# Kernel tuning notes

Measured on AMD Instinct MI355X. Metric: run time of the kernel, lower is better.

The kernel has to match this reference:

```python
import jax, jax.numpy as jnp
import numpy as np

B, LU, LV, D = 16, 2048, 2048, 1024


def setup_inputs() -> dict:
    key = jax.random.key(0)
    ku, kv, kl, kw = jax.random.split(key, 4)
    u = jax.random.normal(ku, (B, LU, D), dtype=jnp.float32)
    v = jax.random.normal(kv, (B, LV, D), dtype=jnp.float32)
    # padding mask: True = masked position; every batch keeps >= LV//2 valid tokens
    lengths = jax.random.randint(kl, (B,), LV // 2, LV + 1)
    v_mask = jnp.arange(LV)[None, :] >= lengths[:, None]  # [B, LV] bool
    # Linear(input_size=D, output_size=D) parameters
    W = jax.random.normal(kw, (D, D), dtype=jnp.float32) * (1.0 / np.sqrt(D))
    b = jnp.zeros((D,), dtype=jnp.float32)
    return {"u": u, "v": v, "v_mask": v_mask, "W": W, "b": b}


def reference(u, v, v_mask, W, b):
    # shared ReLU-projected bilinear attention
    u_ = jax.nn.relu(u @ W.T + b)            # [B, Lu, D]
    v_ = jax.nn.relu(v @ W.T + b)            # [B, Lv, D]
    alpha = jnp.einsum("bud,bvd->buv", u_, v_)  # [B, Lu, Lv]
    alpha = jnp.where(v_mask[:, None, :], -jnp.inf, alpha)
    alpha = jax.nn.softmax(alpha, axis=-1)
    return jnp.einsum("buv,bvd->bud", alpha, v)  # [B, Lu, D]
```

## Files before the change

kernel.cpp:

```cpp
#include <hip/hip_runtime.h>
#include <math.h>

#define B_  16
#define LU_ 2048
#define LV_ 2048
#define D_  1024
#define NT_ (LV_ / 128)
#define MB_ (1024ull * 1024ull)

typedef __attribute__((ext_vector_type(8))) short ush8;
typedef __attribute__((ext_vector_type(8))) _Float16 f16x8;
typedef __attribute__((ext_vector_type(4))) float f32x4;

__device__ __forceinline__ unsigned short f2h(float x) {
    _Float16 h = (_Float16)x;
    return __builtin_bit_cast(unsigned short, h);
}

__device__ __forceinline__ void gload_lds16(const void* g, void* l) {
    __builtin_amdgcn_global_load_lds(
        (const __attribute__((address_space(1))) void*)g,
        (__attribute__((address_space(3))) void*)l, 16, 0, 0);
}

__global__ void lengths_kernel(const void* __restrict__ mask, int* __restrict__ lengths) {
    __shared__ int viol;
    __shared__ int cnt[B_];
    const int t = threadIdx.x;
    if (t == 0) viol = 0;
    if (t < B_) cnt[t] = 0;
    __syncthreads();
    const unsigned char* mb = (const unsigned char*)mask;
    int local = 0;
    for (int i = t; i < B_ * LV_ - 1; i += 256) {
        if (((i + 1) % LV_) != 0) {
            if (mb[i] != 0 && mb[i + 1] == 0) local++;
        }
    }
    if (local) atomicAdd(&viol, local);
    __syncthreads();
    const bool is_i32 = (viol > 0);
    const int b = t >> 4, s = t & 15;
    int c = 0;
    if (is_i32) {
        const int* mi = (const int*)mask;
        for (int v2 = s; v2 < LV_; v2 += 16) c += (mi[b * LV_ + v2] == 0) ? 1 : 0;
    } else {
        for (int v2 = s; v2 < LV_; v2 += 16) c += (mb[b * LV_ + v2] == 0) ? 1 : 0;
    }
    atomicAdd(&cnt[b], c);
    __syncthreads();
    if (t < B_) lengths[t] = cnt[t];
}

__global__ __launch_bounds__(256) void cvt_kernel(
    const float* __restrict__ X, unsigned short* __restrict__ Y, long n8) {
    const long stride = (long)gridDim.x * 256;
    for (long i = (long)blockIdx.x * 256 + threadIdx.x; i < n8; i += stride) {
        float4 x0 = ((const float4*)X)[i * 2];
        float4 x1 = ((const float4*)X)[i * 2 + 1];
        float xv[8] = {x0.x, x0.y, x0.z, x0.w, x1.x, x1.y, x1.z, x1.w};
        ush8 h;
#pragma unroll
        for (int j = 0; j < 8; j++) h[j] = (short)f2h(xv[j]);
        ((ush8*)Y)[i] = h;
    }
}

__global__ __launch_bounds__(256, 2) void proj_kernel(
    const unsigned short* __restrict__ Xf, const unsigned short* __restrict__ Wf,
    const float* __restrict__ bias, const int* __restrict__ lengths, int is_v,
    unsigned short* __restrict__ Yf) {
    if (is_v) {
        const int bb = blockIdx.x >> 4;
        const int lv0 = (blockIdx.x & 15) * 128;
        if (lv0 >= lengths[bb]) return;
    }
    __shared__ alignas(16) unsigned short sA[128 * 64], sB[128 * 64];
    const int t = threadIdx.x, lane = t & 63, w = t >> 6;
    const int fr = lane & 15, fg = lane >> 4;
    const int row0 = blockIdx.x * 128, col0 = blockIdx.y * 128;

    size_t aog[4], bog[4];
    int dbs[4];
#pragma unroll
    for (int i = 0; i < 4; i++) {
        const int r = w * 32 + i * 8 + (lane >> 3);
        const int cg = (lane & 7) ^ (r & 7);
        aog[i] = (size_t)(row0 + r) * D_ + cg * 8;
        bog[i] = (size_t)(col0 + r) * D_ + cg * 8;
        dbs[i] = (w * 32 + i * 8) * 64;
    }
    int aoff[2][2], boff[2][8];
#pragma unroll
    for (int kk = 0; kk < 2; kk++) {
#pragma unroll
        for (int m = 0; m < 2; m++) {
            const int r = w * 32 + m * 16 + fr;
            aoff[kk][m] = r * 64 + (((kk * 4 + fg) ^ (r & 7))) * 8;
        }
#pragma unroll
        for (int n = 0; n < 8; n++) {
            const int r = n * 16 + fr;
            boff[kk][n] = r * 64 + (((kk * 4 + fg) ^ (r & 7))) * 8;
        }
    }

    const f32x4 fzero = {0.f, 0.f, 0.f, 0.f};
    f32x4 acc[2][8];
#pragma unroll
    for (int m = 0; m < 2; m++)
#pragma unroll
        for (int n = 0; n < 8; n++) acc[m][n] = fzero;

#pragma unroll 1
    for (int k0 = 0; k0 < D_; k0 += 64) {
        __syncthreads();
#pragma unroll
        for (int i = 0; i < 4; i++) {
            gload_lds16(Xf + aog[i] + k0, &sA[dbs[i]]);
            gload_lds16(Wf + bog[i] + k0, &sB[dbs[i]]);
        }
        __syncthreads();
#pragma unroll
        for (int kk = 0; kk < 2; kk++) {
            const f16x8 a0 = *(const f16x8*)&sA[aoff[kk][0]];
            const f16x8 a1 = *(const f16x8*)&sA[aoff[kk][1]];
#pragma unroll
            for (int n = 0; n < 8; n++) {
                const f16x8 bv = *(const f16x8*)&sB[boff[kk][n]];
                acc[0][n] = __builtin_amdgcn_mfma_f32_16x16x32_f16(a0, bv, acc[0][n], 0, 0, 0);
                acc[1][n] = __builtin_amdgcn_mfma_f32_16x16x32_f16(a1, bv, acc[1][n], 0, 0, 0);
            }
        }
    }

#pragma unroll
    for (int m = 0; m < 2; m++)
#pragma unroll
        for (int n = 0; n < 8; n++) {
            const int col = col0 + n * 16 + fr;
            const float bv = bias[col];
#pragma unroll
            for (int j = 0; j < 4; j++) {
                const int row = row0 + w * 32 + m * 16 + fg * 4 + j;
                const float y = fmaxf(acc[m][n][j] + bv, 0.f);
                Yf[(size_t)row * D_ + col] = f2h(y);
            }
        }
}

__global__ __launch_bounds__(256) void transpose_v_kernel(
    const float* __restrict__ V, const int* __restrict__ lengths,
    unsigned short* __restrict__ VT, unsigned short* __restrict__ Vraw) {
    __shared__ unsigned short s[64 * 72];
    const int b = blockIdx.z;
    const int v0 = blockIdx.x * 64, d0 = blockIdx.y * 64;
    if (v0 >= ((lengths[b] + 127) & ~127)) return;
    const int t = threadIdx.x;
    {
        const int r = t >> 2, q = (t & 3) * 16;
        const float* src = V + ((size_t)b * LV_ + v0 + r) * D_ + d0 + q;
        unsigned short hb[16];
#pragma unroll
        for (int i = 0; i < 4; i++) {
            float4 x = ((const float4*)src)[i];
            hb[i * 4 + 0] = f2h(x.x);
            hb[i * 4 + 1] = f2h(x.y);
            hb[i * 4 + 2] = f2h(x.z);
            hb[i * 4 + 3] = f2h(x.w);
        }
#pragma unroll
        for (int j = 0; j < 16; j++) s[r * 72 + q + j] = hb[j];
        unsigned short* rdst = Vraw + ((size_t)b * LV_ + v0 + r) * D_ + d0 + q;
        ((ush8*)rdst)[0] = *(ush8*)&hb[0];
        ((ush8*)rdst)[1] = *(ush8*)&hb[8];
    }
    __syncthreads();
    {
        const int d = t >> 2, vq = (t & 3) * 16;
        ush8 t0, t1;
#pragma unroll
        for (int j = 0; j < 8; j++) t0[j] = (short)s[(vq + j) * 72 + d];
#pragma unroll
        for (int j = 0; j < 8; j++) t1[j] = (short)s[(vq + 8 + j) * 72 + d];
        unsigned short* dst = VT + ((size_t)b * D_ + d0 + d) * LV_ + v0 + vq;
        ((ush8*)dst)[0] = t0;
        ((ush8*)dst)[1] = t1;
    }
}

__global__ __launch_bounds__(256, 2) void attn_logits_kernel(
    const unsigned short* __restrict__ Uf, const unsigned short* __restrict__ Vf,
    const int* __restrict__ lengths,
    unsigned short* __restrict__ Pp, float* __restrict__ m_used,
    float* __restrict__ Z_used) {
    __shared__ alignas(16) unsigned short sU[128 * 64], sV[128 * 64];
    const int b = blockIdx.z, ut = blockIdx.x, vt = blockIdx.y;
    const int t = threadIdx.x, lane = t & 63, w = t >> 6;
    const int fr = lane & 15, fg = lane >> 4;
    const int length = lengths[b];
    const int row0 = ut * 128, col0 = vt * 128;

    if (col0 >= length) {
        if (t < 128) {
            const size_t row = (size_t)b * LU_ + row0 + t;
            m_used[row * NT_ + vt] = -__builtin_inff();
            Z_used[row * NT_ + vt] = 0.f;
        }
        return;
    }

    size_t aog[4], bog[4];
    int dbs[4];
#pragma unroll
    for (int i = 0; i < 4; i++) {
        const int r = w * 32 + i * 8 + (lane >> 3);
        const int cg = (lane & 7) ^ (r & 7);
        aog[i] = ((size_t)b * LU_ + row0 + r) * D_ + cg * 8;
        bog[i] = ((size_t)b * LV_ + col0 + r) * D_ + cg * 8;
        dbs[i] = (w * 32 + i * 8) * 64;
    }
    int aoff[2][2], boff[2][8];
#pragma unroll
    for (int kk = 0; kk < 2; kk++) {
#pragma unroll
        for (int m = 0; m < 2; m++) {
            const int r = w * 32 + m * 16 + fr;
            aoff[kk][m] = r * 64 + (((kk * 4 + fg) ^ (r & 7))) * 8;
        }
#pragma unroll
        for (int n = 0; n < 8; n++) {
            const int r = n * 16 + fr;
            boff[kk][n] = r * 64 + (((kk * 4 + fg) ^ (r & 7))) * 8;
        }
    }

    const f32x4 fzero = {0.f, 0.f, 0.f, 0.f};
    f32x4 acc[2][8];
#pragma unroll
    for (int m = 0; m < 2; m++)
#pragma unroll
        for (int n = 0; n < 8; n++) acc[m][n] = fzero;

#pragma unroll 1
    for (int k0 = 0; k0 < D_; k0 += 64) {
        __syncthreads();
#pragma unroll
        for (int i = 0; i < 4; i++) {
            gload_lds16(Uf + aog[i] + k0, &sU[dbs[i]]);
            gload_lds16(Vf + bog[i] + k0, &sV[dbs[i]]);
        }
        __syncthreads();
#pragma unroll
        for (int kk = 0; kk < 2; kk++) {
            const f16x8 a0 = *(const f16x8*)&sU[aoff[kk][0]];
            const f16x8 a1 = *(const f16x8*)&sU[aoff[kk][1]];
#pragma unroll
            for (int n = 0; n < 8; n++) {
                const f16x8 bv = *(const f16x8*)&sV[boff[kk][n]];
                acc[0][n] = __builtin_amdgcn_mfma_f32_16x16x32_f16(a0, bv, acc[0][n], 0, 0, 0);
                acc[1][n] = __builtin_amdgcn_mfma_f32_16x16x32_f16(a1, bv, acc[1][n], 0, 0, 0);
            }
        }
    }

#pragma unroll
    for (int m = 0; m < 2; m++) {
        float mt[4] = {-__builtin_inff(), -__builtin_inff(), -__builtin_inff(), -__builtin_inff()};
#pragma unroll
        for (int n = 0; n < 8; n++) {
            const int col = col0 + n * 16 + fr;
            if (col < length) {
#pragma unroll
                for (int j = 0; j < 4; j++) mt[j] = fmaxf(mt[j], acc[m][n][j]);
            }
        }
#pragma unroll
        for (int d = 1; d < 16; d <<= 1) {
#pragma unroll
            for (int j = 0; j < 4; j++) mt[j] = fmaxf(mt[j], __shfl_xor(mt[j], d));
        }
        float rs[4] = {0.f, 0.f, 0.f, 0.f};
#pragma unroll
        for (int n = 0; n < 8; n++) {
            const int col = col0 + n * 16 + fr;
            const bool valid = (col < length);
#pragma unroll
            for (int j = 0; j < 4; j++) {
                const float p = valid ? __expf(acc[m][n][j] - mt[j]) : 0.f;
                rs[j] += p;
                const size_t row = (size_t)b * LU_ + row0 + w * 32 + m * 16 + fg * 4 + j;
                Pp[row * LV_ + col] = f2h(p);
            }
        }
#pragma unroll
        for (int d = 1; d < 16; d <<= 1) {
#pragma unroll
            for (int j = 0; j < 4; j++) rs[j] += __shfl_xor(rs[j], d);
        }
        if (fr == 0) {
#pragma unroll
            for (int j = 0; j < 4; j++) {
                const size_t row = (size_t)b * LU_ + row0 + w * 32 + m * 16 + fg * 4 + j;
                m_used[row * NT_ + vt] = mt[j];
                Z_used[row * NT_ + vt] = rs[j];
            }
        }
    }
}

__global__ __launch_bounds__(256, 4) void pv_gemm_kernel(
    const unsigned short* __restrict__ Pp, const unsigned short* __restrict__ VT,
    const float* __restrict__ m_used, const float* __restrict__ Z_used,
    const int* __restrict__ lengths, float* __restrict__ Out) {
    __shared__ alignas(16) unsigned short sA[128 * 64], sB[128 * 64];
    __shared__ float sSc[NT_ * 128];
    const int b = blockIdx.z, bm = blockIdx.x, bn = blockIdx.y;
    const int t = threadIdx.x, lane = t & 63, w = t >> 6;
    const int wr = (w >> 1) * 64, wc = (w & 1) * 64;
    const int fr = lane & 15, fg = lane >> 4;
    const int length = lengths[b];
    const int ntv = (length + 127) >> 7;

    if (t < 128) {
        const size_t row = (size_t)b * LU_ + bm * 128 + t;
        float mv[NT_];
        float m = -__builtin_inff();
#pragma unroll
        for (int i = 0; i < NT_; i++) {
            mv[i] = m_used[row * NT_ + i];
            m = fmaxf(m, mv[i]);
        }
        float ev[NT_];
        float z = 0.f;
#pragma unroll
        for (int i = 0; i < NT_; i++) {
            ev[i] = __expf(mv[i] - m);
            z += Z_used[row * NT_ + i] * ev[i];
        }
        const float inv = 1.f / z;
#pragma unroll
        for (int i = 0; i < NT_; i++) sSc[i * 128 + t] = ev[i] * inv;
    }
    __syncthreads();

    size_t aog[4], bog[4];
    int dbs[4];
#pragma unroll
    for (int i = 0; i < 4; i++) {
        const int r = w * 32 + i * 8 + (lane >> 3);
        const int cg = (lane & 7) ^ (r & 7);
        aog[i] = ((size_t)b * LU_ + bm * 128 + r) * LV_ + cg * 8;
        bog[i] = ((size_t)b * D_ + bn * 128 + r) * LV_ + cg * 8;
        dbs[i] = (w * 32 + i * 8) * 64;
    }
    int aoff[2][4], boff[2][4];
#pragma unroll
    for (int kk = 0; kk < 2; kk++) {
#pragma unroll
        for (int m = 0; m < 4; m++) {
            const int r = wr + m * 16 + fr;
            aoff[kk][m] = r * 64 + (((kk * 4 + fg) ^ (r & 7))) * 8;
        }
#pragma unroll
        for (int n = 0; n < 4; n++) {
            const int r = wc + n * 16 + fr;
            boff[kk][n] = r * 64 + (((kk * 4 + fg) ^ (r & 7))) * 8;
        }
    }

    const f32x4 fzero = {0.f, 0.f, 0.f, 0.f};
    f32x4 acc[4][4];
#pragma unroll
    for (int m = 0; m < 4; m++)
#pragma unroll
        for (int n = 0; n < 4; n++) acc[m][n] = fzero;

#pragma unroll 1
    for (int vt = 0; vt < ntv; ++vt) {
        f16x8 scv[4];
#pragma unroll
        for (int m = 0; m < 4; m++) {
            const _Float16 sh = (_Float16)sSc[vt * 128 + wr + m * 16 + fr];
#pragma unroll
            for (int j = 0; j < 8; j++) scv[m][j] = sh;
        }

#pragma unroll 1
        for (int kb = 0; kb < 2; ++kb) {
            const int k0 = vt * 128 + kb * 64;
            __syncthreads();
#pragma unroll
            for (int i = 0; i < 4; i++) {
                gload_lds16(Pp + aog[i] + k0, &sA[dbs[i]]);
                gload_lds16(VT + bog[i] + k0, &sB[dbs[i]]);
            }
            __syncthreads();
#pragma unroll
            for (int kk = 0; kk < 2; kk++) {
                f16x8 af[4];
#pragma unroll
                for (int m = 0; m < 4; m++)
                    af[m] = (*(const f16x8*)&sA[aoff[kk][m]]) * scv[m];
#pragma unroll
                for (int n = 0; n < 4; n++) {
                    const f16x8 bv = *(const f16x8*)&sB[boff[kk][n]];
#pragma unroll
                    for (int m = 0; m < 4; m++)
                        acc[m][n] = __builtin_amdgcn_mfma_f32_16x16x32_f16(af[m], bv, acc[m][n], 0, 0, 0);
                }
            }
        }
    }

    float* Ob = Out + (size_t)b * LU_ * D_;
#pragma unroll
    for (int m = 0; m < 4; m++) {
        const int rbase = bm * 128 + wr + m * 16 + fg * 4;
#pragma unroll
        for (int n = 0; n < 4; n++) {
            const int col = bn * 128 + wc + n * 16 + fr;
#pragma unroll
            for (int j = 0; j < 4; j++)
                Ob[(size_t)(rbase + j) * D_ + col] = acc[m][n][j];
        }
    }
}

extern "C" void kernel_launch(void* const* d_in, const int* in_sizes, int n_in,
                              void* d_out, int out_size, void* d_ws, size_t ws_size,
                              hipStream_t stream) {
    (void)in_sizes; (void)n_in; (void)out_size; (void)ws_size;
    const float* u    = (const float*)d_in[0];
    const float* v    = (const float*)d_in[1];
    const void*  vm   = d_in[2];
    const float* W    = (const float*)d_in[3];
    const float* bias = (const float*)d_in[4];
    float* out = (float*)d_out;
    char* ws = (char*)d_ws;

    unsigned short* Pp    = (unsigned short*)(ws + 0 * MB_);
    unsigned short* vT    = (unsigned short*)(ws + 128 * MB_);
    unsigned short* u_f   = (unsigned short*)(ws + 192 * MB_);
    unsigned short* v_f   = (unsigned short*)(ws + 256 * MB_);
    unsigned short* vraw  = (unsigned short*)(ws + 320 * MB_);
    unsigned short* xs_u  = (unsigned short*)(ws + 384 * MB_);
    unsigned short* W_f   = (unsigned short*)(ws + 448 * MB_);
    int*   lengths = (int*)(ws + 450 * MB_);
    float* m_used  = (float*)(ws + 451 * MB_);
    float* Z_used  = (float*)(ws + 453 * MB_);

    const long nW8 = (long)D_ * D_ / 8;
    const long nX8 = (long)B_ * LU_ * D_ / 8;

    lengths_kernel<<<1, 256, 0, stream>>>(vm, lengths);
    cvt_kernel<<<512, 256, 0, stream>>>(W, W_f, nW8);
    cvt_kernel<<<4096, 256, 0, stream>>>(u, xs_u, nX8);
    proj_kernel<<<dim3(B_ * LU_ / 128, D_ / 128), 256, 0, stream>>>(
        xs_u, W_f, bias, lengths, 0, u_f);
    transpose_v_kernel<<<dim3(LV_ / 64, D_ / 64, B_), 256, 0, stream>>>(v, lengths, vT, vraw);
    proj_kernel<<<dim3(B_ * LV_ / 128, D_ / 128), 256, 0, stream>>>(
        vraw, W_f, bias, lengths, 1, v_f);
    attn_logits_kernel<<<dim3(LU_ / 128, NT_, B_), 256, 0, stream>>>(
        u_f, v_f, lengths, Pp, m_used, Z_used);
    pv_gemm_kernel<<<dim3(LU_ / 128, D_ / 128, B_), 256, 0, stream>>>(
        Pp, vT, m_used, Z_used, lengths, out);
}
```

Before: 575.3 us.

## Use 256x256 tiles, 512 threads and double-buffered LDS prefetch in all GEMMs

The projection, logits and PV GEMM kernels move from 128x128 tiles with 256 threads to 256x256 tiles with 512 threads (8 waves, each computing a 128x64 sub-tile). Each kernel now double-buffers A/B tiles in dynamic LDS (128 KB or more), prefetching two k-steps ahead with global_load_lds. It waits on vmcnt, syncs with raw s_barrier, and raises wave priority around the MFMA block. Bigger tiles are meant to raise data reuse and cut global traffic, and the prefetch is meant to hide load latency behind MFMA. The softmax statistics in the logits kernel are now reduced across 4 column-waves through LDS, giving 8 partial (max, sum) pairs per row instead of 16. The cost is large LDS use and high register pressure, which limits occupancy to about one block per CU.

```diff
diff --git a/kernel.cpp b/kernel.cpp
--- a/kernel.cpp
+++ b/kernel.cpp
@@ -5,7 +5,7 @@
 #define LU_ 2048
 #define LV_ 2048
 #define D_  1024
-#define NT_ (LV_ / 128)
+#define NTC_ 8
 #define MB_ (1024ull * 1024ull)
 
 typedef __attribute__((ext_vector_type(8))) short ush8;
@@ -21,6 +21,12 @@
     __builtin_amdgcn_global_load_lds(
         (const __attribute__((address_space(1))) void*)g,
         (__attribute__((address_space(3))) void*)l, 16, 0, 0);
+}
+
+__device__ __forceinline__ void raw_barrier() {
+    asm volatile("" ::: "memory");
+    __builtin_amdgcn_s_barrier();
+    asm volatile("" ::: "memory");
 }
 
 __global__ void lengths_kernel(const void* __restrict__ mask, int* __restrict__ lengths) {
@@ -67,19 +73,23 @@
     }
 }
 
-__global__ __launch_bounds__(256, 2) void proj_kernel(
+
+__global__ __launch_bounds__(512, 2) void proj_kernel(
     const unsigned short* __restrict__ Xf, const unsigned short* __restrict__ Wf,
     const float* __restrict__ bias, const int* __restrict__ lengths, int is_v,
     unsigned short* __restrict__ Yf) {
     if (is_v) {
-        const int bb = blockIdx.x >> 4;
-        const int lv0 = (blockIdx.x & 15) * 128;
+        const int bb = blockIdx.x >> 3;
+        const int lv0 = (blockIdx.x & 7) * 256;
         if (lv0 >= lengths[bb]) return;
     }
-    __shared__ alignas(16) unsigned short sA[128 * 64], sB[128 * 64];
+    extern __shared__ unsigned short lds[];
+    unsigned short* sA = lds;
+    unsigned short* sB = lds + 32768;
     const int t = threadIdx.x, lane = t & 63, w = t >> 6;
+    const int wm = w >> 2, wn = w & 3;
     const int fr = lane & 15, fg = lane >> 4;
-    const int row0 = blockIdx.x * 128, col0 = blockIdx.y * 128;
+    const int row0 = blockIdx.x * 256, col0 = blockIdx.y * 256;
 
     size_t aog[4], bog[4];
     int dbs[4];
@@ -91,63 +101,86 @@
         bog[i] = (size_t)(col0 + r) * D_ + cg * 8;
         dbs[i] = (w * 32 + i * 8) * 64;
     }
-    int aoff[2][2], boff[2][8];
+    int aoff[2][8], boff[2][4];
 #pragma unroll
     for (int kk = 0; kk < 2; kk++) {
 #pragma unroll
-        for (int m = 0; m < 2; m++) {
-            const int r = w * 32 + m * 16 + fr;
+        for (int m = 0; m < 8; m++) {
+            const int r = wm * 128 + m * 16 + fr;
             aoff[kk][m] = r * 64 + (((kk * 4 + fg) ^ (r & 7))) * 8;
         }
 #pragma unroll
-        for (int n = 0; n < 8; n++) {
-            const int r = n * 16 + fr;
+        for (int n = 0; n < 4; n++) {
+            const int r = wn * 64 + n * 16 + fr;
             boff[kk][n] = r * 64 + (((kk * 4 + fg) ^ (r & 7))) * 8;
         }
     }
 
     const f32x4 fzero = {0.f, 0.f, 0.f, 0.f};
-    f32x4 acc[2][8];
-#pragma unroll
-    for (int m = 0; m < 2; m++)
-#pragma unroll
-        for (int n = 0; n < 8; n++) acc[m][n] = fzero;
+    f32x4 acc[8][4];
+#pragma unroll
+    for (int m = 0; m < 8; m++)
+#pragma unroll
+        for (int n = 0; n < 4; n++) acc[m][n] = fzero;
+
+    const int NKT = D_ / 64;
+#pragma unroll
+    for (int i = 0; i < 4; i++) {
+        gload_lds16(Xf + aog[i], &sA[dbs[i]]);
+        gload_lds16(Wf + bog[i], &sB[dbs[i]]);
+    }
+#pragma unroll
+    for (int i = 0; i < 4; i++) {
+        gload_lds16(Xf + aog[i] + 64, &sA[16384 + dbs[i]]);
+        gload_lds16(Wf + bog[i] + 64, &sB[16384 + dbs[i]]);
+    }
 
 #pragma unroll 1
-    for (int k0 = 0; k0 < D_; k0 += 64) {
-        __syncthreads();
-#pragma unroll
-        for (int i = 0; i < 4; i++) {
-            gload_lds16(Xf + aog[i] + k0, &sA[dbs[i]]);
-            gload_lds16(Wf + bog[i] + k0, &sB[dbs[i]]);
-        }
-        __syncthreads();
+    for (int tk = 0; tk < NKT; ++tk) {
+        const int d = (tk & 1) * 16384;
+        if (tk < NKT - 1) asm volatile("s_waitcnt vmcnt(8)" ::: "memory");
+        else              asm volatile("s_waitcnt vmcnt(0)" ::: "memory");
+        raw_barrier();
 #pragma unroll
         for (int kk = 0; kk < 2; kk++) {
-            const f16x8 a0 = *(const f16x8*)&sA[aoff[kk][0]];
-            const f16x8 a1 = *(const f16x8*)&sA[aoff[kk][1]];
-#pragma unroll
-            for (int n = 0; n < 8; n++) {
-                const f16x8 bv = *(const f16x8*)&sB[boff[kk][n]];
-                acc[0][n] = __builtin_amdgcn_mfma_f32_16x16x32_f16(a0, bv, acc[0][n], 0, 0, 0);
-                acc[1][n] = __builtin_amdgcn_mfma_f32_16x16x32_f16(a1, bv, acc[1][n], 0, 0, 0);
+            f16x8 av[8], bv[4];
+#pragma unroll
+            for (int m = 0; m < 8; m++) av[m] = *(const f16x8*)&sA[d + aoff[kk][m]];
+#pragma unroll
+            for (int n = 0; n < 4; n++) bv[n] = *(const f16x8*)&sB[d + boff[kk][n]];
+            __builtin_amdgcn_s_setprio(1);
+#pragma unroll
+            for (int m = 0; m < 8; m++)
+#pragma unroll
+                for (int n = 0; n < 4; n++)
+                    acc[m][n] = __builtin_amdgcn_mfma_f32_16x16x32_f16(av[m], bv[n], acc[m][n], 0, 0, 0);
+            __builtin_amdgcn_s_setprio(0);
+        }
+        raw_barrier();
+        if (tk + 2 < NKT) {
+            const size_t ka = (size_t)(tk + 2) * 64;
+#pragma unroll
+            for (int i = 0; i < 4; i++) {
+                gload_lds16(Xf + aog[i] + ka, &sA[d + dbs[i]]);
+                gload_lds16(Wf + bog[i] + ka, &sB[d + dbs[i]]);
             }
         }
     }
 
 #pragma unroll
-    for (int m = 0; m < 2; m++)
-#pragma unroll
-        for (int n = 0; n < 8; n++) {
-            const int col = col0 + n * 16 + fr;
-            const float bv = bias[col];
+    for (int n = 0; n < 4; n++) {
+        const int col = col0 + wn * 64 + n * 16 + fr;
+        const float bv = bias[col];
+#pragma unroll
+        for (int m = 0; m < 8; m++) {
 #pragma unroll
             for (int j = 0; j < 4; j++) {
-                const int row = row0 + w * 32 + m * 16 + fg * 4 + j;
+                const int row = row0 + wm * 128 + m * 16 + fg * 4 + j;
                 const float y = fmaxf(acc[m][n][j] + bv, 0.f);
                 Yf[(size_t)row * D_ + col] = f2h(y);
             }
         }
+    }
 }
 
 __global__ __launch_bounds__(256) void transpose_v_kernel(
@@ -190,23 +223,26 @@
     }
 }
 
-__global__ __launch_bounds__(256, 2) void attn_logits_kernel(
+__global__ __launch_bounds__(512, 2) void attn_logits_kernel(
     const unsigned short* __restrict__ Uf, const unsigned short* __restrict__ Vf,
     const int* __restrict__ lengths,
     unsigned short* __restrict__ Pp, float* __restrict__ m_used,
     float* __restrict__ Z_used) {
-    __shared__ alignas(16) unsigned short sU[128 * 64], sV[128 * 64];
-    const int b = blockIdx.z, ut = blockIdx.x, vt = blockIdx.y;
+    extern __shared__ unsigned short lds[];
+    unsigned short* sA = lds;
+    unsigned short* sB = lds + 32768;
+    const int b = blockIdx.z, ut = blockIdx.x, vty = blockIdx.y;
     const int t = threadIdx.x, lane = t & 63, w = t >> 6;
+    const int wm = w >> 2, wn = w & 3;
     const int fr = lane & 15, fg = lane >> 4;
     const int length = lengths[b];
-    const int row0 = ut * 128, col0 = vt * 128;
+    const int row0 = ut * 256, col0 = vty * 256;
 
     if (col0 >= length) {
-        if (t < 128) {
+        if (t < 256) {
             const size_t row = (size_t)b * LU_ + row0 + t;
-            m_used[row * NT_ + vt] = -__builtin_inff();
-            Z_used[row * NT_ + vt] = 0.f;
+            m_used[row * NTC_ + vty] = -__builtin_inff();
+            Z_used[row * NTC_ + vty] = 0.f;
         }
         return;
     }
@@ -221,127 +257,175 @@
         bog[i] = ((size_t)b * LV_ + col0 + r) * D_ + cg * 8;
         dbs[i] = (w * 32 + i * 8) * 64;
     }
-    int aoff[2][2], boff[2][8];
+    int aoff[2][8], boff[2][4];
 #pragma unroll
     for (int kk = 0; kk < 2; kk++) {
 #pragma unroll
-        for (int m = 0; m < 2; m++) {
-            const int r = w * 32 + m * 16 + fr;
+        for (int m = 0; m < 8; m++) {
+            const int r = wm * 128 + m * 16 + fr;
             aoff[kk][m] = r * 64 + (((kk * 4 + fg) ^ (r & 7))) * 8;
         }
 #pragma unroll
-        for (int n = 0; n < 8; n++) {
-            const int r = n * 16 + fr;
+        for (int n = 0; n < 4; n++) {
+            const int r = wn * 64 + n * 16 + fr;
             boff[kk][n] = r * 64 + (((kk * 4 + fg) ^ (r & 7))) * 8;
         }
     }
 
     const f32x4 fzero = {0.f, 0.f, 0.f, 0.f};
-    f32x4 acc[2][8];
-#pragma unroll
-    for (int m = 0; m < 2; m++)
-#pragma unroll
-        for (int n = 0; n < 8; n++) acc[m][n] = fzero;
+    f32x4 acc[8][4];
+#pragma unroll
+    for (int m = 0; m < 8; m++)
+#pragma unroll
+        for (int n = 0; n < 4; n++) acc[m][n] = fzero;
+
+    const int NKT = D_ / 64;
+#pragma unroll
+    for (int i = 0; i < 4; i++) {
+        gload_lds16(Uf + aog[i], &sA[dbs[i]]);
+        gload_lds16(Vf + bog[i], &sB[dbs[i]]);
+    }
+#pragma unroll
+    for (int i = 0; i < 4; i++) {
+        gload_lds16(Uf + aog[i] + 64, &sA[16384 + dbs[i]]);
+        gload_lds16(Vf + bog[i] + 64, &sB[16384 + dbs[i]]);
+    }
 
 #pragma unroll 1
-    for (int k0 = 0; k0 < D_; k0 += 64) {
-        __syncthreads();
-#pragma unroll
-        for (int i = 0; i < 4; i++) {
-            gload_lds16(Uf + aog[i] + k0, &sU[dbs[i]]);
-            gload_lds16(Vf + bog[i] + k0, &sV[dbs[i]]);
-        }
-        __syncthreads();
+    for (int tk = 0; tk < NKT; ++tk) {
+        const int d = (tk & 1) * 16384;
+        if (tk < NKT - 1) asm volatile("s_waitcnt vmcnt(8)" ::: "memory");
+        else              asm volatile("s_waitcnt vmcnt(0)" ::: "memory");
+        raw_barrier();
 #pragma unroll
         for (int kk = 0; kk < 2; kk++) {
-            const f16x8 a0 = *(const f16x8*)&sU[aoff[kk][0]];
-            const f16x8 a1 = *(const f16x8*)&sU[aoff[kk][1]];
-#pragma unroll
-            for (int n = 0; n < 8; n++) {
-                const f16x8 bv = *(const f16x8*)&sV[boff[kk][n]];
-                acc[0][n] = __builtin_amdgcn_mfma_f32_16x16x32_f16(a0, bv, acc[0][n], 0, 0, 0);
-                acc[1][n] = __builtin_amdgcn_mfma_f32_16x16x32_f16(a1, bv, acc[1][n], 0, 0, 0);
+            f16x8 av[8], bv[4];
+#pragma unroll
+            for (int m = 0; m < 8; m++) av[m] = *(const f16x8*)&sA[d + aoff[kk][m]];
+#pragma unroll
+            for (int n = 0; n < 4; n++) bv[n] = *(const f16x8*)&sB[d + boff[kk][n]];
+            __builtin_amdgcn_s_setprio(1);
+#pragma unroll
+            for (int m = 0; m < 8; m++)
+#pragma unroll
+                for (int n = 0; n < 4; n++)
+                    acc[m][n] = __builtin_amdgcn_mfma_f32_16x16x32_f16(av[m], bv[n], acc[m][n], 0, 0, 0);
+            __builtin_amdgcn_s_setprio(0);
+        }
+        raw_barrier();
+        if (tk + 2 < NKT) {
+            const size_t ka = (size_t)(tk + 2) * 64;
+#pragma unroll
+            for (int i = 0; i < 4; i++) {
+                gload_lds16(Uf + aog[i] + ka, &sA[d + dbs[i]]);
+                gload_lds16(Vf + bog[i] + ka, &sB[d + dbs[i]]);
             }
         }
     }
 
-#pragma unroll
-    for (int m = 0; m < 2; m++) {
+    __syncthreads();
+    float* sMax = (float*)lds;
+    float* sSum = sMax + 1024;
+#pragma unroll
+    for (int m = 0; m < 8; m++) {
         float mt[4] = {-__builtin_inff(), -__builtin_inff(), -__builtin_inff(), -__builtin_inff()};
 #pragma unroll
-        for (int n = 0; n < 8; n++) {
-            const int col = col0 + n * 16 + fr;
+        for (int n = 0; n < 4; n++) {
+            const int col = col0 + wn * 64 + n * 16 + fr;
             if (col < length) {
 #pragma unroll
                 for (int j = 0; j < 4; j++) mt[j] = fmaxf(mt[j], acc[m][n][j]);
             }
         }
 #pragma unroll
-        for (int d = 1; d < 16; d <<= 1) {
-#pragma unroll
-            for (int j = 0; j < 4; j++) mt[j] = fmaxf(mt[j], __shfl_xor(mt[j], d));
-        }
-        float rs[4] = {0.f, 0.f, 0.f, 0.f};
-#pragma unroll
-        for (int n = 0; n < 8; n++) {
-            const int col = col0 + n * 16 + fr;
+        for (int dd = 1; dd < 16; dd <<= 1) {
+#pragma unroll
+            for (int j = 0; j < 4; j++) mt[j] = fmaxf(mt[j], __shfl_xor(mt[j], dd));
+        }
+        if (fr == 0) {
+#pragma unroll
+            for (int j = 0; j < 4; j++)
+                sMax[(wm * 128 + m * 16 + fg * 4 + j) * 4 + wn] = mt[j];
+        }
+    }
+    __syncthreads();
+#pragma unroll
+    for (int m = 0; m < 8; m++) {
+        float mrow[4], rs[4] = {0.f, 0.f, 0.f, 0.f};
+#pragma unroll
+        for (int j = 0; j < 4; j++) {
+            const int rl = wm * 128 + m * 16 + fg * 4 + j;
+            mrow[j] = fmaxf(fmaxf(sMax[rl * 4 + 0], sMax[rl * 4 + 1]),
+                            fmaxf(sMax[rl * 4 + 2], sMax[rl * 4 + 3]));
+        }
+#pragma unroll
+        for (int n = 0; n < 4; n++) {
+            const int col = col0 + wn * 64 + n * 16 + fr;
             const bool valid = (col < length);
 #pragma unroll
             for (int j = 0; j < 4; j++) {
-                const float p = valid ? __expf(acc[m][n][j] - mt[j]) : 0.f;
+                const float p = valid ? __expf(acc[m][n][j] - mrow[j]) : 0.f;
                 rs[j] += p;
-                const size_t row = (size_t)b * LU_ + row0 + w * 32 + m * 16 + fg * 4 + j;
+                const size_t row = (size_t)b * LU_ + row0 + wm * 128 + m * 16 + fg * 4 + j;
                 Pp[row * LV_ + col] = f2h(p);
             }
         }
 #pragma unroll
-        for (int d = 1; d < 16; d <<= 1) {
-#pragma unroll
-            for (int j = 0; j < 4; j++) rs[j] += __shfl_xor(rs[j], d);
+        for (int dd = 1; dd < 16; dd <<= 1) {
+#pragma unroll
+            for (int j = 0; j < 4; j++) rs[j] += __shfl_xor(rs[j], dd);
         }
         if (fr == 0) {
 #pragma unroll
-            for (int j = 0; j < 4; j++) {
-                const size_t row = (size_t)b * LU_ + row0 + w * 32 + m * 16 + fg * 4 + j;
-                m_used[row * NT_ + vt] = mt[j];
-                Z_used[row * NT_ + vt] = rs[j];
-            }
-        }
-    }
-}
-
-__global__ __launch_bounds__(256, 4) void pv_gemm_kernel(
+            for (int j = 0; j < 4; j++)
+                sSum[(wm * 128 + m * 16 + fg * 4 + j) * 4 + wn] = rs[j];
+        }
+    }
+    __syncthreads();
+    if (t < 256) {
+        const float m_t = fmaxf(fmaxf(sMax[t * 4 + 0], sMax[t * 4 + 1]),
+                                fmaxf(sMax[t * 4 + 2], sMax[t * 4 + 3]));
+        const float z = sSum[t * 4 + 0] + sSum[t * 4 + 1] + sSum[t * 4 + 2] + sSum[t * 4 + 3];
+        const size_t row = (size_t)b * LU_ + row0 + t;
+        m_used[row * NTC_ + vty] = m_t;
+        Z_used[row * NTC_ + vty] = z;
+    }
+}
+
+__global__ __launch_bounds__(512, 2) void pv_gemm_kernel(
     const unsigned short* __restrict__ Pp, const unsigned short* __restrict__ VT,
     const float* __restrict__ m_used, const float* __restrict__ Z_used,
     const int* __restrict__ lengths, float* __restrict__ Out) {
-    __shared__ alignas(16) unsigned short sA[128 * 64], sB[128 * 64];
-    __shared__ float sSc[NT_ * 128];
+    extern __shared__ unsigned short lds[];
+    unsigned short* sA = lds;
+    unsigned short* sB = lds + 32768;
+    float* sSc = (float*)(lds + 65536);
     const int b = blockIdx.z, bm = blockIdx.x, bn = blockIdx.y;
     const int t = threadIdx.x, lane = t & 63, w = t >> 6;
-    const int wr = (w >> 1) * 64, wc = (w & 1) * 64;
+    const int wm = w >> 2, wn = w & 3;
     const int fr = lane & 15, fg = lane >> 4;
     const int length = lengths[b];
-    const int ntv = (length + 127) >> 7;
-
-    if (t < 128) {
-        const size_t row = (size_t)b * LU_ + bm * 128 + t;
-        float mv[NT_];
+    const int nkt = ((length + 127) >> 7) * 2;
+
+    if (t < 256) {
+        const size_t row = (size_t)b * LU_ + bm * 256 + t;
+        float mv[NTC_];
         float m = -__builtin_inff();
 #pragma unroll
-        for (int i = 0; i < NT_; i++) {
-            mv[i] = m_used[row * NT_ + i];
+        for (int i = 0; i < NTC_; i++) {
+            mv[i] = m_used[row * NTC_ + i];
             m = fmaxf(m, mv[i]);
         }
-        float ev[NT_];
         float z = 0.f;
-#pragma unroll
-        for (int i = 0; i < NT_; i++) {
+        float ev[NTC_];
+#pragma unroll
+        for (int i = 0; i < NTC_; i++) {
             ev[i] = __expf(mv[i] - m);
-            z += Z_used[row * NT_ + i] * ev[i];
+            z += Z_used[row * NTC_ + i] * ev[i];
         }
         const float inv = 1.f / z;
 #pragma unroll
-        for (int i = 0; i < NT_; i++) sSc[i * 128 + t] = ev[i] * inv;
+        for (int i = 0; i < NTC_; i++) sSc[i * 256 + t] = ev[i] * inv;
     }
     __syncthreads();
 
@@ -351,76 +435,88 @@
     for (int i = 0; i < 4; i++) {
         const int r = w * 32 + i * 8 + (lane >> 3);
         const int cg = (lane & 7) ^ (r & 7);
-        aog[i] = ((size_t)b * LU_ + bm * 128 + r) * LV_ + cg * 8;
-        bog[i] = ((size_t)b * D_ + bn * 128 + r) * LV_ + cg * 8;
+        aog[i] = ((size_t)b * LU_ + bm * 256 + r) * LV_ + cg * 8;
+        bog[i] = ((size_t)b * D_ + bn * 256 + r) * LV_ + cg * 8;
         dbs[i] = (w * 32 + i * 8) * 64;
     }
-    int aoff[2][4], boff[2][4];
+    int aoff[2][8], boff[2][4];
 #pragma unroll
     for (int kk = 0; kk < 2; kk++) {
 #pragma unroll
-        for (int m = 0; m < 4; m++) {
-            const int r = wr + m * 16 + fr;
+        for (int m = 0; m < 8; m++) {
+            const int r = wm * 128 + m * 16 + fr;
             aoff[kk][m] = r * 64 + (((kk * 4 + fg) ^ (r & 7))) * 8;
         }
 #pragma unroll
         for (int n = 0; n < 4; n++) {
-            const int r = wc + n * 16 + fr;
+            const int r = wn * 64 + n * 16 + fr;
             boff[kk][n] = r * 64 + (((kk * 4 + fg) ^ (r & 7))) * 8;
         }
     }
 
     const f32x4 fzero = {0.f, 0.f, 0.f, 0.f};
-    f32x4 acc[4][4];
-#pragma unroll
-    for (int m = 0; m < 4; m++)
+    f32x4 acc[8][4];
+#pragma unroll
+    for (int m = 0; m < 8; m++)
 #pragma unroll
         for (int n = 0; n < 4; n++) acc[m][n] = fzero;
 
+#pragma unroll
+    for (int i = 0; i < 4; i++) {
+        gload_lds16(Pp + aog[i], &sA[dbs[i]]);
+        gload_lds16(VT + bog[i], &sB[dbs[i]]);
+    }
+#pragma unroll
+    for (int i = 0; i < 4; i++) {
+        gload_lds16(Pp + aog[i] + 64, &sA[16384 + dbs[i]]);
+        gload_lds16(VT + bog[i] + 64, &sB[16384 + dbs[i]]);
+    }
+
 #pragma unroll 1
-    for (int vt = 0; vt < ntv; ++vt) {
-        f16x8 scv[4];
-#pragma unroll
-        for (int m = 0; m < 4; m++) {
-            const _Float16 sh = (_Float16)sSc[vt * 128 + wr + m * 16 + fr];
-#pragma unroll
-            for (int j = 0; j < 8; j++) scv[m][j] = sh;
-        }
-
-#pragma unroll 1
-        for (int kb = 0; kb < 2; ++kb) {
-            const int k0 = vt * 128 + kb * 64;
-            __syncthreads();
+    for (int tk = 0; tk < nkt; ++tk) {
+        const int d = (tk & 1) * 16384;
+        const int vt256 = tk >> 2;
+        _Float16 scv[8];
+#pragma unroll
+        for (int m = 0; m < 8; m++)
+            scv[m] = (_Float16)sSc[vt256 * 256 + wm * 128 + m * 16 + fr];
+        if (tk < nkt - 1) asm volatile("s_waitcnt vmcnt(8)" ::: "memory");
+        else              asm volatile("s_waitcnt vmcnt(0)" ::: "memory");
+        raw_barrier();
+#pragma unroll
+        for (int kk = 0; kk < 2; kk++) {
+            f16x8 av[8], bv[4];
+#pragma unroll
+            for (int m = 0; m < 8; m++)
+                av[m] = (*(const f16x8*)&sA[d + aoff[kk][m]]) * scv[m];
+#pragma unroll
+            for (int n = 0; n < 4; n++) bv[n] = *(const f16x8*)&sB[d + boff[kk][n]];
+            __builtin_amdgcn_s_setprio(1);
+#pragma unroll
+            for (int m = 0; m < 8; m++)
+#pragma unroll
+                for (int n = 0; n < 4; n++)
+                    acc[m][n] = __builtin_amdgcn_mfma_f32_16x16x32_f16(av[m], bv[n], acc[m][n], 0, 0, 0);
+            __builtin_amdgcn_s_setprio(0);
+        }
+        raw_barrier();
+        if (tk + 2 < nkt) {
+            const size_t ka = (size_t)(tk + 2) * 64;
 #pragma unroll
             for (int i = 0; i < 4; i++) {
-                gload_lds16(Pp + aog[i] + k0, &sA[dbs[i]]);
-                gload_lds16(VT + bog[i] + k0, &sB[dbs[i]]);
+                gload_lds16(Pp + aog[i] + ka, &sA[d + dbs[i]]);
+                gload_lds16(VT + bog[i] + ka, &sB[d + dbs[i]]);
             }
-            __syncthreads();
-#pragma unroll
-            for (int kk = 0; kk < 2; kk++) {
-                f16x8 af[4];
-#pragma unroll
-                for (int m = 0; m < 4; m++)
-                    af[m] = (*(const f16x8*)&sA[aoff[kk][m]]) * scv[m];
-#pragma unroll
-                for (int n = 0; n < 4; n++) {
-                    const f16x8 bv = *(const f16x8*)&sB[boff[kk][n]];
-#pragma unroll
-                    for (int m = 0; m < 4; m++)
-                        acc[m][n] = __builtin_amdgcn_mfma_f32_16x16x32_f16(af[m], bv, acc[m][n], 0, 0, 0);
-                }
-            }
         }
     }
 
     float* Ob = Out + (size_t)b * LU_ * D_;
 #pragma unroll
-    for (int m = 0; m < 4; m++) {
-        const int rbase = bm * 128 + wr + m * 16 + fg * 4;
+    for (int m = 0; m < 8; m++) {
+        const int rbase = bm * 256 + wm * 128 + m * 16 + fg * 4;
 #pragma unroll
         for (int n = 0; n < 4; n++) {
-            const int col = bn * 128 + wc + n * 16 + fr;
+            const int col = bn * 256 + wn * 64 + n * 16 + fr;
 #pragma unroll
             for (int j = 0; j < 4; j++)
                 Ob[(size_t)(rbase + j) * D_ + col] = acc[m][n][j];
@@ -453,17 +549,19 @@
 
     const long nW8 = (long)D_ * D_ / 8;
     const long nX8 = (long)B_ * LU_ * D_ / 8;
+    const size_t LDSB  = 131072;
+    const size_t LDSBP = 139264;
 
     lengths_kernel<<<1, 256, 0, stream>>>(vm, lengths);
     cvt_kernel<<<512, 256, 0, stream>>>(W, W_f, nW8);
     cvt_kernel<<<4096, 256, 0, stream>>>(u, xs_u, nX8);
-    proj_kernel<<<dim3(B_ * LU_ / 128, D_ / 128), 256, 0, stream>>>(
+    proj_kernel<<<dim3(B_ * LU_ / 256, D_ / 256), 512, LDSB, stream>>>(
         xs_u, W_f, bias, lengths, 0, u_f);
     transpose_v_kernel<<<dim3(LV_ / 64, D_ / 64, B_), 256, 0, stream>>>(v, lengths, vT, vraw);
-    proj_kernel<<<dim3(B_ * LV_ / 128, D_ / 128), 256, 0, stream>>>(
+    proj_kernel<<<dim3(B_ * LV_ / 256, D_ / 256), 512, LDSB, stream>>>(
         vraw, W_f, bias, lengths, 1, v_f);
-    attn_logits_kernel<<<dim3(LU_ / 128, NT_, B_), 256, 0, stream>>>(
+    attn_logits_kernel<<<dim3(LU_ / 256, LV_ / 256, B_), 512, LDSB, stream>>>(
         u_f, v_f, lengths, Pp, m_used, Z_used);
-    pv_gemm_kernel<<<dim3(LU_ / 128, D_ / 128, B_), 256, 0, stream>>>(
+    pv_gemm_kernel<<<dim3(LU_ / 256, D_ / 256, B_), 512, LDSBP, stream>>>(
         Pp, vT, m_used, Z_used, lengths, out);
 }
```

Result: slower. 646.6 us (+12.4%).
